# Kernel optimization log

Hardware: AMD Instinct MI355X
Metric: run time of the kernel (lower is better)

Reference implementation:

```python
import jax, jax.numpy as jnp
import numpy as np

B, T, D = 32, 2048, 128


def setup_inputs() -> dict:
    key = jax.random.key(0)
    k1, k2, k3 = jax.random.split(key, 3)
    values = jax.random.normal(k1, (B, T, D), dtype=jnp.float32)
    # monotonically increasing per-feature timestamps (irregular sampling)
    times = jnp.cumsum(jax.random.uniform(k2, (B, T, D), dtype=jnp.float32), axis=1)
    mask = jax.random.randint(k3, (B, T, D), 0, 2) > 0  # True = observed
    return {"values": values, "times": times, "mask": mask}


def _fill(x, t, mask):
    """Parallel forward fill (LOCF) and backward fill (NOCB) of x and t.

    Replaces the serial Keras RNN scan with cummax/cummin over observation
    indices followed by a gather. Matches ForwardCell semantics:
      forward : x init 0, t init times[:, 0, :]
      backward: x init 0, t init max(times, axis=1)
    """
    Tn = x.shape[1]
    ar = jnp.broadcast_to(jnp.arange(Tn, dtype=jnp.int32)[None, :, None], x.shape)
    # ---- forward fill ----
    fidx = jax.lax.cummax(jnp.where(mask, ar, -1), axis=1)  # last observed idx
    fvalid = fidx >= 0
    fi = jnp.clip(fidx, 0, Tn - 1)
    x_last = jnp.where(fvalid, jnp.take_along_axis(x, fi, axis=1), 0.0)
    t_last = jnp.where(fvalid, jnp.take_along_axis(t, fi, axis=1), t[:, :1, :])
    # ---- backward fill ----
    bidx = jax.lax.cummin(jnp.where(mask, ar, Tn), axis=1, reverse=True)  # next observed idx
    bvalid = bidx < Tn
    bi = jnp.clip(bidx, 0, Tn - 1)
    x_next = jnp.where(bvalid, jnp.take_along_axis(x, bi, axis=1), 0.0)
    t_next = jnp.where(bvalid, jnp.take_along_axis(t, bi, axis=1),
                       jnp.max(t, axis=1, keepdims=True))
    return x_last, t_last, x_next, t_next


def reference(values, times, mask):
    x_last, t_last, x_next, t_next = _fill(values, times, mask)
    denom = t_next - t_last
    num = x_last * (t_next - times) + x_next * (times - t_last)
    safe = denom != 0.0
    x_itp = num / jnp.where(safe, denom, 1.0)
    x_itp = jnp.where(safe & jnp.isfinite(x_itp), x_itp, 0.0)  # nan/inf -> 0
    return jnp.where(mask, values, x_itp)
```

## Files before the change

### kernel.cpp

```cpp
#include <hip/hip_runtime.h>
#include <math.h>

constexpr int B  = 32;
constexpr int T  = 2048;
constexpr int D  = 128;
constexpr int CS = 8;
constexpr int RT = 8;
constexpr int BT = RT * CS;
constexpr int DQ = 32;

__global__ __launch_bounds__(256)
void interp_wave_kernel(const float* __restrict__ values,
                        const float* __restrict__ times,
                        const int*   __restrict__ mask,
                        float*       __restrict__ out)
{
    const int tid  = threadIdx.x;
    const int lane = tid & 63;
    const int row  = lane >> 3;
    const int dg   = lane & 7;
    const int waveId = (blockIdx.x << 2) + (tid >> 6);
    const int dq = waveId & 3;
    const int tb = (waveId >> 2) & 31;
    const int b  = waveId >> 7;

    const int d0  = dq * DQ + dg * 4;
    const int bt0 = tb * BT;
    const int t0  = bt0 + row * CS;

    const size_t bbase = (size_t)b * T * D;
    const float* vrow = values + bbase + (size_t)t0 * D + d0;
    const float* trow = times  + bbase + (size_t)t0 * D + d0;
    const int*   mrow = mask   + bbase + (size_t)t0 * D + d0;

    float vv[CS][4], tt[CS][4];
    unsigned mb[4] = {0u, 0u, 0u, 0u};
#pragma unroll
    for (int i = 0; i < CS; ++i) {
        const float4 a = *reinterpret_cast<const float4*>(vrow + i * D);
        const float4 s = *reinterpret_cast<const float4*>(trow + i * D);
        const int4   m = *reinterpret_cast<const int4*>(mrow + i * D);
        vv[i][0] = a.x; vv[i][1] = a.y; vv[i][2] = a.z; vv[i][3] = a.w;
        tt[i][0] = s.x; tt[i][1] = s.y; tt[i][2] = s.z; tt[i][3] = s.w;
        mb[0] |= (m.x != 0 ? 1u : 0u) << i;
        mb[1] |= (m.y != 0 ? 1u : 0u) << i;
        mb[2] |= (m.z != 0 ? 1u : 0u) << i;
        mb[3] |= (m.w != 0 ? 1u : 0u) << i;
    }

    unsigned pbp0 = 0u, pbp1 = 0u;
    unsigned nbp0 = 0u, nbp1 = 0u;
    if (row == 0 && tb > 0) {
#pragma unroll
        for (int k = 0; k < 16; ++k) {
            const int4 m = *reinterpret_cast<const int4*>(
                mask + bbase + (size_t)(bt0 - 16 + k) * D + d0);
            pbp0 |= (m.x != 0 ? 1u : 0u) << k;
            pbp0 |= (m.y != 0 ? 1u : 0u) << (16 + k);
            pbp1 |= (m.z != 0 ? 1u : 0u) << k;
            pbp1 |= (m.w != 0 ? 1u : 0u) << (16 + k);
        }
    }
    if (row == RT - 1 && tb < 31) {
#pragma unroll
        for (int k = 0; k < 16; ++k) {
            const int4 m = *reinterpret_cast<const int4*>(
                mask + bbase + (size_t)(bt0 + BT + k) * D + d0);
            nbp0 |= (m.x != 0 ? 1u : 0u) << k;
            nbp0 |= (m.y != 0 ? 1u : 0u) << (16 + k);
            nbp1 |= (m.z != 0 ? 1u : 0u) << k;
            nbp1 |= (m.w != 0 ? 1u : 0u) << (16 + k);
        }
    }

    float lv[4], lt[4], fv[4], ftm[4];
#pragma unroll
    for (int j = 0; j < 4; ++j) {
        float a = 0.f, c = 0.f, e = 0.f, g = 0.f;
#pragma unroll
        for (int i = 0; i < CS; ++i)
            if ((mb[j] >> i) & 1u) { a = vv[i][j]; c = tt[i][j]; }
#pragma unroll
        for (int i = CS - 1; i >= 0; --i)
            if ((mb[j] >> i) & 1u) { e = vv[i][j]; g = tt[i][j]; }
        lv[j] = a; lt[j] = c; fv[j] = e; ftm[j] = g;
    }
    const unsigned smP = (mb[0] & 0xFFu) | ((mb[1] & 0xFFu) << 8)
                       | ((mb[2] & 0xFFu) << 16) | ((mb[3] & 0xFFu) << 24);

    unsigned allm[RT];
#pragma unroll
    for (int r = 0; r < RT; ++r)
        allm[r] = (unsigned)__shfl((int)smP, r * 8 + dg, 64);
    const unsigned pbs0 = (unsigned)__shfl((int)pbp0, dg, 64);
    const unsigned pbs1 = (unsigned)__shfl((int)pbp1, dg, 64);
    const unsigned nbs0 = (unsigned)__shfl((int)nbp0, 56 + dg, 64);
    const unsigned nbs1 = (unsigned)__shfl((int)nbp1, 56 + dg, 64);

#pragma unroll
    for (int j = 0; j < 4; ++j) {
        const int d = d0 + j;
        unsigned rm = 0u;
#pragma unroll
        for (int r = 0; r < RT; ++r)
            rm |= (((allm[r] >> (8 * j)) & 0xFFu) ? 1u : 0u) << r;

        const unsigned below = rm & ((1u << row) - 1u);
        const unsigned above = rm >> (row + 1);

        const int rs = below ? (31 - __builtin_clz(below)) : 0;
        const int rb = above ? (row + 1 + __builtin_ctz(above)) : 0;
        const float gLV = __shfl(lv[j],  rs * 8 + dg, 64);
        const float gLT = __shfl(lt[j],  rs * 8 + dg, 64);
        const float gFV = __shfl(fv[j],  rb * 8 + dg, 64);
        const float gFT = __shfl(ftm[j], rb * 8 + dg, 64);

        float cfx, cft;
        if (below) { cfx = gLV; cft = gLT; }
        else {
            const unsigned pbj = ((j & 1) ? ((j < 2 ? pbs0 : pbs1) >> 16)
                                          :  (j < 2 ? pbs0 : pbs1)) & 0xFFFFu;
            if (pbj) {
                const int st = bt0 - 16 + (31 - __builtin_clz(pbj));
                const size_t o = bbase + (size_t)st * D + d;
                cfx = values[o]; cft = times[o];
            } else {
                bool found = false; cfx = 0.f; cft = 0.f;
                for (int st = bt0 - 17; st >= 0; --st) {
                    if (mask[bbase + (size_t)st * D + d] != 0) {
                        const size_t o = bbase + (size_t)st * D + d;
                        cfx = values[o]; cft = times[o]; found = true; break;
                    }
                }
                if (!found) { cfx = 0.f; cft = times[bbase + d]; }
            }
        }

        float cbx, cbt;
        if (above) { cbx = gFV; cbt = gFT; }
        else {
            const unsigned nbj = ((j & 1) ? ((j < 2 ? nbs0 : nbs1) >> 16)
                                          :  (j < 2 ? nbs0 : nbs1)) & 0xFFFFu;
            if (nbj) {
                const int st = bt0 + BT + __builtin_ctz(nbj);
                const size_t o = bbase + (size_t)st * D + d;
                cbx = values[o]; cbt = times[o];
            } else {
                bool found = false; cbx = 0.f; cbt = 0.f;
                for (int st = bt0 + BT + 16; st < T; ++st) {
                    if (mask[bbase + (size_t)st * D + d] != 0) {
                        const size_t o = bbase + (size_t)st * D + d;
                        cbx = values[o]; cbt = times[o]; found = true; break;
                    }
                }
                if (!found) { cbx = 0.f; cbt = times[bbase + (size_t)(T - 1) * D + d]; }
            }
        }

        float xl[CS], tl_[CS];
#pragma unroll
        for (int i = 0; i < CS; ++i) {
            if ((mb[j] >> i) & 1u) { cfx = vv[i][j]; cft = tt[i][j]; }
            xl[i] = cfx; tl_[i] = cft;
        }
#pragma unroll
        for (int i = CS - 1; i >= 0; --i) {
            const bool obs = (mb[j] >> i) & 1u;
            if (obs) { cbx = vv[i][j]; cbt = tt[i][j]; }
            const float denom = cbt - tl_[i];
            const float num   = xl[i] * (cbt - tt[i][j]) + cbx * (tt[i][j] - tl_[i]);
            const bool  safe  = (denom != 0.f);
            float xi = num / (safe ? denom : 1.f);
            xi = (safe && isfinite(xi)) ? xi : 0.f;
            vv[i][j] = obs ? vv[i][j] : xi;
        }
    }

    float* orow = out + bbase + (size_t)t0 * D + d0;
#pragma unroll
    for (int i = 0; i < CS; ++i) {
        float4 o; o.x = vv[i][0]; o.y = vv[i][1]; o.z = vv[i][2]; o.w = vv[i][3];
        *reinterpret_cast<float4*>(orow + i * D) = o;
    }
}

extern "C" void kernel_launch(void* const* d_in, const int* in_sizes, int n_in,
                              void* d_out, int out_size, void* d_ws, size_t ws_size,
                              hipStream_t stream)
{
    const float* values = (const float*)d_in[0];
    const float* times  = (const float*)d_in[1];
    const int*   mask   = (const int*)d_in[2];
    float*       out    = (float*)d_out;

    const int blocks = (B * (T / BT) * (D / DQ)) / 4;
    interp_wave_kernel<<<blocks, 256, 0, stream>>>(values, times, mask, out);
}
```

Baseline: 154.6 us.

## Remap wave to 16 time-groups × 16 features and use ballots for halo masks

Each wave now covers 64 timesteps by 16 features, with 4 timesteps per lane instead of 8. This halves per-thread register arrays and doubles the number of waves. Cross-lane observation masks and the ±16-step halo masks are built with wave ballots instead of shuffle gathers and serial 16-row loads by edge lanes. All lanes now share the halo loads, and ballot bit-scans replace the per-row mask assembly. Memory traffic per element stays the same, and feature contiguity per row drops to 64 bytes per group.

```diff
diff --git a/kernel.cpp b/kernel.cpp
--- a/kernel.cpp
+++ b/kernel.cpp
@@ -4,29 +4,30 @@
 constexpr int B  = 32;
 constexpr int T  = 2048;
 constexpr int D  = 128;
-constexpr int CS = 8;
-constexpr int RT = 8;
-constexpr int BT = RT * CS;
-constexpr int DQ = 32;
+constexpr int CS = 4;
+constexpr int GW = 16;
+constexpr int WT = GW * CS;
+constexpr int WD = 16;
 
 __global__ __launch_bounds__(256)
-void interp_wave_kernel(const float* __restrict__ values,
-                        const float* __restrict__ times,
-                        const int*   __restrict__ mask,
-                        float*       __restrict__ out)
+void interp_ballot_kernel(const float* __restrict__ values,
+                          const float* __restrict__ times,
+                          const int*   __restrict__ mask,
+                          float*       __restrict__ out)
 {
     const int tid  = threadIdx.x;
     const int lane = tid & 63;
-    const int row  = lane >> 3;
-    const int dg   = lane & 7;
-    const int waveId = (blockIdx.x << 2) + (tid >> 6);
-    const int dq = waveId & 3;
-    const int tb = (waveId >> 2) & 31;
-    const int b  = waveId >> 7;
+    const int g    = lane >> 2;
+    const int q    = lane & 3;
 
-    const int d0  = dq * DQ + dg * 4;
-    const int bt0 = tb * BT;
-    const int t0  = bt0 + row * CS;
+    const int waveId = (blockIdx.x << 2) | (tid >> 6);
+    const int db   = waveId & 7;
+    const int tile = (waveId >> 3) & 31;
+    const int b    = waveId >> 8;
+
+    const int d0  = db * WD + q * 4;
+    const int bt0 = tile * WT;
+    const int t0  = bt0 + g * CS;
 
     const size_t bbase = (size_t)b * T * D;
     const float* vrow = values + bbase + (size_t)t0 * D + d0;
@@ -48,80 +49,64 @@
         mb[3] |= (m.w != 0 ? 1u : 0u) << i;
     }
 
-    unsigned pbp0 = 0u, pbp1 = 0u;
-    unsigned nbp0 = 0u, nbp1 = 0u;
-    if (row == 0 && tb > 0) {
-#pragma unroll
-        for (int k = 0; k < 16; ++k) {
-            const int4 m = *reinterpret_cast<const int4*>(
-                mask + bbase + (size_t)(bt0 - 16 + k) * D + d0);
-            pbp0 |= (m.x != 0 ? 1u : 0u) << k;
-            pbp0 |= (m.y != 0 ? 1u : 0u) << (16 + k);
-            pbp1 |= (m.z != 0 ? 1u : 0u) << k;
-            pbp1 |= (m.w != 0 ? 1u : 0u) << (16 + k);
-        }
+    unsigned long long hpb[4] = {0ull, 0ull, 0ull, 0ull};
+    unsigned long long hnb[4] = {0ull, 0ull, 0ull, 0ull};
+    if (tile > 0) {
+        const int4 m = *reinterpret_cast<const int4*>(
+            mask + bbase + (size_t)(bt0 - 16 + g) * D + db * WD + q * 4);
+        hpb[0] = __ballot(m.x != 0);
+        hpb[1] = __ballot(m.y != 0);
+        hpb[2] = __ballot(m.z != 0);
+        hpb[3] = __ballot(m.w != 0);
     }
-    if (row == RT - 1 && tb < 31) {
-#pragma unroll
-        for (int k = 0; k < 16; ++k) {
-            const int4 m = *reinterpret_cast<const int4*>(
-                mask + bbase + (size_t)(bt0 + BT + k) * D + d0);
-            nbp0 |= (m.x != 0 ? 1u : 0u) << k;
-            nbp0 |= (m.y != 0 ? 1u : 0u) << (16 + k);
-            nbp1 |= (m.z != 0 ? 1u : 0u) << k;
-            nbp1 |= (m.w != 0 ? 1u : 0u) << (16 + k);
-        }
+    if (tile < 31) {
+        const int4 m = *reinterpret_cast<const int4*>(
+            mask + bbase + (size_t)(bt0 + WT + g) * D + db * WD + q * 4);
+        hnb[0] = __ballot(m.x != 0);
+        hnb[1] = __ballot(m.y != 0);
+        hnb[2] = __ballot(m.z != 0);
+        hnb[3] = __ballot(m.w != 0);
     }
 
     float lv[4], lt[4], fv[4], ftm[4];
 #pragma unroll
     for (int j = 0; j < 4; ++j) {
-        float a = 0.f, c = 0.f, e = 0.f, g = 0.f;
+        float a = 0.f, c = 0.f, e = 0.f, h = 0.f;
 #pragma unroll
         for (int i = 0; i < CS; ++i)
             if ((mb[j] >> i) & 1u) { a = vv[i][j]; c = tt[i][j]; }
 #pragma unroll
         for (int i = CS - 1; i >= 0; --i)
-            if ((mb[j] >> i) & 1u) { e = vv[i][j]; g = tt[i][j]; }
-        lv[j] = a; lt[j] = c; fv[j] = e; ftm[j] = g;
+            if ((mb[j] >> i) & 1u) { e = vv[i][j]; h = tt[i][j]; }
+        lv[j] = a; lt[j] = c; fv[j] = e; ftm[j] = h;
     }
-    const unsigned smP = (mb[0] & 0xFFu) | ((mb[1] & 0xFFu) << 8)
-                       | ((mb[2] & 0xFFu) << 16) | ((mb[3] & 0xFFu) << 24);
 
-    unsigned allm[RT];
+    unsigned long long gb[4];
 #pragma unroll
-    for (int r = 0; r < RT; ++r)
-        allm[r] = (unsigned)__shfl((int)smP, r * 8 + dg, 64);
-    const unsigned pbs0 = (unsigned)__shfl((int)pbp0, dg, 64);
-    const unsigned pbs1 = (unsigned)__shfl((int)pbp1, dg, 64);
-    const unsigned nbs0 = (unsigned)__shfl((int)nbp0, 56 + dg, 64);
-    const unsigned nbs1 = (unsigned)__shfl((int)nbp1, 56 + dg, 64);
+    for (int j = 0; j < 4; ++j)
+        gb[j] = __ballot(mb[j] != 0u);
+    const unsigned long long colmask = 0x1111111111111111ull << q;
 
 #pragma unroll
     for (int j = 0; j < 4; ++j) {
         const int d = d0 + j;
-        unsigned rm = 0u;
-#pragma unroll
-        for (int r = 0; r < RT; ++r)
-            rm |= (((allm[r] >> (8 * j)) & 0xFFu) ? 1u : 0u) << r;
+        const unsigned long long col   = gb[j] & colmask;
+        const unsigned long long below = col & ((1ull << lane) - 1ull);
+        const unsigned long long above = col & ~((2ull << lane) - 1ull);
 
-        const unsigned below = rm & ((1u << row) - 1u);
-        const unsigned above = rm >> (row + 1);
-
-        const int rs = below ? (31 - __builtin_clz(below)) : 0;
-        const int rb = above ? (row + 1 + __builtin_ctz(above)) : 0;
-        const float gLV = __shfl(lv[j],  rs * 8 + dg, 64);
-        const float gLT = __shfl(lt[j],  rs * 8 + dg, 64);
-        const float gFV = __shfl(fv[j],  rb * 8 + dg, 64);
-        const float gFT = __shfl(ftm[j], rb * 8 + dg, 64);
+        const int rsF = below ? (63 - __builtin_clzll(below)) : lane;
+        const int rsB = above ? __builtin_ctzll(above) : lane;
+        const float gLV = __shfl(lv[j],  rsF, 64);
+        const float gLT = __shfl(lt[j],  rsF, 64);
+        const float gFV = __shfl(fv[j],  rsB, 64);
+        const float gFT = __shfl(ftm[j], rsB, 64);
 
         float cfx, cft;
         if (below) { cfx = gLV; cft = gLT; }
         else {
-            const unsigned pbj = ((j & 1) ? ((j < 2 ? pbs0 : pbs1) >> 16)
-                                          :  (j < 2 ? pbs0 : pbs1)) & 0xFFFFu;
-            if (pbj) {
-                const int st = bt0 - 16 + (31 - __builtin_clz(pbj));
+            const unsigned long long hcol = hpb[j] & colmask;
+            if (hcol) {
+                const int st = bt0 - 16 + ((63 - __builtin_clzll(hcol)) >> 2);
                 const size_t o = bbase + (size_t)st * D + d;
                 cfx = values[o]; cft = times[o];
             } else {
@@ -139,15 +124,14 @@
         float cbx, cbt;
         if (above) { cbx = gFV; cbt = gFT; }
         else {
-            const unsigned nbj = ((j & 1) ? ((j < 2 ? nbs0 : nbs1) >> 16)
-                                          :  (j < 2 ? nbs0 : nbs1)) & 0xFFFFu;
-            if (nbj) {
-                const int st = bt0 + BT + __builtin_ctz(nbj);
+            const unsigned long long hcol = hnb[j] & colmask;
+            if (hcol) {
+                const int st = bt0 + WT + (__builtin_ctzll(hcol) >> 2);
                 const size_t o = bbase + (size_t)st * D + d;
                 cbx = values[o]; cbt = times[o];
             } else {
                 bool found = false; cbx = 0.f; cbt = 0.f;
-                for (int st = bt0 + BT + 16; st < T; ++st) {
+                for (int st = bt0 + WT + 16; st < T; ++st) {
                     if (mask[bbase + (size_t)st * D + d] != 0) {
                         const size_t o = bbase + (size_t)st * D + d;
                         cbx = values[o]; cbt = times[o]; found = true; break;
@@ -193,6 +177,6 @@
     const int*   mask   = (const int*)d_in[2];
     float*       out    = (float*)d_out;
 
-    const int blocks = (B * (T / BT) * (D / DQ)) / 4;
-    interp_wave_kernel<<<blocks, 256, 0, stream>>>(values, times, mask, out);
+    const int blocks = (B * (T / WT) * (D / WD) * 64) / 256;
+    interp_ballot_kernel<<<blocks, 256, 0, stream>>>(values, times, mask, out);
 }
```

Measured after the change: 136.2 us. 11.9% less time.
